# Kernel tuning notes

Hardware: AMD Instinct MI355X
Metric: run time of the kernel (lower is better)

Reference implementation:

```python
import jax, jax.numpy as jnp
import numpy as np


def _radon(img, angles, nBins):
    """Parallel-beam forward projection of a single [n, n] image.

    For each angle theta and detector bin s, integrate along the ray
    p = s*(cos,sin) + t*(-sin,cos) using bilinear interpolation with
    zero outside the image. Step size = 1 pixel, nSteps = n.
    Returns sinogram [nViews, nBins].
    """
    n = img.shape[-1]
    c = (n - 1) / 2.0
    s = jnp.arange(nBins, dtype=jnp.float32) - (nBins - 1) / 2.0  # detector coords
    t = jnp.arange(n, dtype=jnp.float32) - (n - 1) / 2.0          # integration param

    def samp(xi, yi):
        valid = (xi >= 0) & (xi < n) & (yi >= 0) & (yi < n)
        xi = jnp.clip(xi, 0, n - 1)
        yi = jnp.clip(yi, 0, n - 1)
        return jnp.where(valid, img[yi, xi], 0.0)

    def per_angle(theta):
        ct, st = jnp.cos(theta), jnp.sin(theta)
        # sample coordinates [nBins, nSteps]
        x = s[:, None] * ct - t[None, :] * st + c
        y = s[:, None] * st + t[None, :] * ct + c
        x0 = jnp.floor(x)
        y0 = jnp.floor(y)
        wx = x - x0
        wy = y - y0
        x0i = x0.astype(jnp.int32)
        y0i = y0.astype(jnp.int32)
        v = (samp(x0i, y0i) * (1 - wx) * (1 - wy)
             + samp(x0i + 1, y0i) * wx * (1 - wy)
             + samp(x0i, y0i + 1) * (1 - wx) * wy
             + samp(x0i + 1, y0i + 1) * wx * wy)
        return v.sum(axis=1)  # ray integral -> [nBins]

    # lax.map over angles keeps per-angle interpolation buffers small
    return jax.lax.map(per_angle, angles)  # [nViews, nBins]


def setup_inputs() -> dict:
    key = jax.random.key(0)
    x = jax.random.normal(key, (4, 1, 512, 512), dtype=jnp.float32)
    return {"x": x, "nViews": 512, "nBins": 512}


def reference(x, nViews, nBins):
    angles = jnp.arange(nViews, dtype=jnp.float32) * (np.pi / nViews)
    img = x[:, 0]  # [B, n, n]
    sino = jax.vmap(lambda im: _radon(im, angles, nBins))(img)  # [B, nViews, nBins]
    return sino[:, None, :, :]
```

## Files before the change

kernel.cpp:

```cpp
#include <hip/hip_runtime.h>


#define N_IMG 512
#define N_VIEWS 512
#define N_BINS 512
#define SB 64
#define TC 32
#define NCH (N_IMG / TC)
#define TDY 76
#define TDX 80
#define PITCH 81
#define GPR (TDX / 4)
#define NGRAN (TDY * GPR)

__global__ __launch_bounds__(256) void radon_fp_tiled4(const float* __restrict__ img,
                                                       float* __restrict__ out) {
    __shared__ float tile[TDY * PITCH];
    __shared__ float red[4][SB];

    const int v     = blockIdx.x;
    const int b     = blockIdx.y;
    const int stile = blockIdx.z;
    const int tid   = threadIdx.x;
    const int binl  = tid & 63;
    const int g     = tid >> 6;

    const float dth = (float)(3.14159265358979323846 / (double)N_VIEWS);
    float st, ct;
    sincosf((float)v * dth, &st, &ct);

    const float c = (float)(N_IMG - 1) * 0.5f;
    const float s = (float)(stile * SB + binl) - (float)(N_BINS - 1) * 0.5f;

    const float* __restrict__ im = img + (size_t)b * (N_IMG * N_IMG);

    const float sA  = (float)(stile * SB) - (float)(N_BINS - 1) * 0.5f;
    const float sBv = sA + (float)(SB - 1);

    float acc = 0.0f;

    for (int ch = 0; ch < NCH; ++ch) {
        const float tA = (float)(ch * TC) - (float)(N_IMG - 1) * 0.5f;
        const float tB = tA + (float)(TC - 1);

        const float xs[4] = { sA * ct - tA * st, sA * ct - tB * st,
                              sBv * ct - tA * st, sBv * ct - tB * st };
        const float ys[4] = { sA * st + tA * ct, sA * st + tB * ct,
                              sBv * st + tA * ct, sBv * st + tB * ct };
        const float xmin = fminf(fminf(xs[0], xs[1]), fminf(xs[2], xs[3])) + c;
        const float ymin = fminf(fminf(ys[0], ys[1]), fminf(ys[2], ys[3])) + c;
        const int X0 = ((int)floorf(xmin) - 1) & ~3;
        const int Y0 = (int)floorf(ymin) - 1;

        __syncthreads();

        const bool interior = (X0 >= 0) & (X0 + TDX <= N_IMG) &
                              (Y0 >= 0) & (Y0 + TDY <= N_IMG);
        if (interior) {
#pragma unroll
            for (int k = 0; k < 6; ++k) {
                const int gi = tid + k * 256;
                if (k < 5 || gi < NGRAN) {
                    const int r  = gi / GPR;
                    const int c4 = (gi - r * GPR) * 4;
                    const float4 vv = *reinterpret_cast<const float4*>(
                        im + ((Y0 + r) << 9) + X0 + c4);
                    float* dst = &tile[r * PITCH + c4];
                    dst[0] = vv.x; dst[1] = vv.y; dst[2] = vv.z; dst[3] = vv.w;
                }
            }
        } else {
#pragma unroll
            for (int k = 0; k < 6; ++k) {
                const int gi = tid + k * 256;
                if (k < 5 || gi < NGRAN) {
                    const int r  = gi / GPR;
                    const int c4 = (gi - r * GPR) * 4;
                    const int gy = Y0 + r;
                    const bool rowok = ((unsigned)gy < (unsigned)N_IMG);
                    float* dst = &tile[r * PITCH + c4];
#pragma unroll
                    for (int q = 0; q < 4; ++q) {
                        const int gx = X0 + c4 + q;
                        float val = 0.0f;
                        if (rowok && (unsigned)gx < (unsigned)N_IMG)
                            val = im[(gy << 9) + gx];
                        dst[q] = val;
                    }
                }
            }
        }
        __syncthreads();

        const float xbase = fmaf(s, ct, c - (float)X0);
        const float ybase = fmaf(s, st, c - (float)Y0);
        const float tb0 = (float)(ch * TC + g * 8) - (float)(N_IMG - 1) * 0.5f;
        const float xg = fmaf(-tb0, st, xbase);
        const float yg = fmaf(tb0, ct, ybase);
#pragma unroll
        for (int j = 0; j < 8; ++j) {
            const float xl = fmaf(-(float)j, st, xg);
            const float yl = fmaf((float)j, ct, yg);
            const float x0 = floorf(xl);
            const float y0 = floorf(yl);
            const float wx = xl - x0;
            const float wy = yl - y0;
            const int e = (int)fmaf(y0, (float)PITCH, x0);
            const float* p = &tile[e];
            const float v00 = p[0];
            const float v10 = p[1];
            const float v01 = p[PITCH];
            const float v11 = p[PITCH + 1];
            const float a0 = fmaf(v10 - v00, wx, v00);
            const float a1 = fmaf(v11 - v01, wx, v01);
            acc += fmaf(a1 - a0, wy, a0);
        }
    }

    red[g][binl] = acc;
    __syncthreads();
    if (tid < SB) {
        const float r0 = red[0][tid] + red[1][tid] + red[2][tid] + red[3][tid];
        out[((size_t)(b * N_VIEWS + v) << 9) + stile * SB + tid] = r0;
    }
}

extern "C" void kernel_launch(void* const* d_in, const int* in_sizes, int n_in,
                              void* d_out, int out_size, void* d_ws, size_t ws_size,
                              hipStream_t stream) {
    const float* img = (const float*)d_in[0];
    float* out = (float*)d_out;
    const int B = in_sizes[0] / (N_IMG * N_IMG);
    dim3 grid(N_VIEWS, B, N_BINS / SB);
    radon_fp_tiled4<<<grid, 256, 0, stream>>>(img, out);
}
```

Before: 688.8 us.

## Remap threads to 2D bin-by-step patches and reduce with wave shuffles

Each wavefront now covers 16 bins by 8 step offsets: a lane handles two bins, 8 apart, and strided steps, instead of one bin with 8 consecutive steps. This keeps a wave's LDS gathers within a compact 2D footprint, which is meant to cut LDS bank conflicts and add ILP through two independent accumulators. The final reduction uses cross-lane shuffles instead of a shared-memory array and an extra barrier. The tile-load index math is also simplified into fixed row/column splits with no division. The new thread mapping makes the access pattern depend on angle in a different way, which could help some views and hurt others.

```diff
diff --git a/kernel.cpp b/kernel.cpp
--- a/kernel.cpp
+++ b/kernel.cpp
@@ -10,34 +10,38 @@
 #define TDY 76
 #define TDX 80
 #define PITCH 81
-#define GPR (TDX / 4)
-#define NGRAN (TDY * GPR)
 
-__global__ __launch_bounds__(256) void radon_fp_tiled4(const float* __restrict__ img,
+__global__ __launch_bounds__(256) void radon_fp_tiled5(const float* __restrict__ img,
                                                        float* __restrict__ out) {
     __shared__ float tile[TDY * PITCH];
-    __shared__ float red[4][SB];
 
     const int v     = blockIdx.x;
     const int b     = blockIdx.y;
     const int stile = blockIdx.z;
     const int tid   = threadIdx.x;
-    const int binl  = tid & 63;
-    const int g     = tid >> 6;
+    const int lane  = tid & 63;
+    const int w     = tid >> 6;
+    const int ls    = lane & 7;
+    const int lt    = lane >> 3;
 
     const float dth = (float)(3.14159265358979323846 / (double)N_VIEWS);
     float st, ct;
     sincosf((float)v * dth, &st, &ct);
 
     const float c = (float)(N_IMG - 1) * 0.5f;
-    const float s = (float)(stile * SB + binl) - (float)(N_BINS - 1) * 0.5f;
+    const float s0 = (float)(stile * SB + w * 16 + ls) - (float)(N_BINS - 1) * 0.5f;
 
     const float* __restrict__ im = img + (size_t)b * (N_IMG * N_IMG);
 
     const float sA  = (float)(stile * SB) - (float)(N_BINS - 1) * 0.5f;
     const float sBv = sA + (float)(SB - 1);
 
-    float acc = 0.0f;
+    const int rA = tid >> 4;
+    const int gA = tid & 15;
+    const int rB = tid >> 2;
+    const int gB = 16 + (tid & 3);
+
+    float acc0 = 0.0f, acc1 = 0.0f;
 
     for (int ch = 0; ch < NCH; ++ch) {
         const float tA = (float)(ch * TC) - (float)(N_IMG - 1) * 0.5f;
@@ -58,30 +62,53 @@
                               (Y0 >= 0) & (Y0 + TDY <= N_IMG);
         if (interior) {
 #pragma unroll
-            for (int k = 0; k < 6; ++k) {
-                const int gi = tid + k * 256;
-                if (k < 5 || gi < NGRAN) {
-                    const int r  = gi / GPR;
-                    const int c4 = (gi - r * GPR) * 4;
+            for (int k = 0; k < 5; ++k) {
+                const int r = rA + k * 16;
+                if (k < 4 || r < TDY) {
                     const float4 vv = *reinterpret_cast<const float4*>(
-                        im + ((Y0 + r) << 9) + X0 + c4);
-                    float* dst = &tile[r * PITCH + c4];
+                        im + ((Y0 + r) << 9) + X0 + 4 * gA);
+                    float* dst = &tile[r * PITCH + 4 * gA];
+                    dst[0] = vv.x; dst[1] = vv.y; dst[2] = vv.z; dst[3] = vv.w;
+                }
+            }
+#pragma unroll
+            for (int k = 0; k < 2; ++k) {
+                const int r = rB + k * 64;
+                if (k == 0 || r < TDY) {
+                    const float4 vv = *reinterpret_cast<const float4*>(
+                        im + ((Y0 + r) << 9) + X0 + 4 * gB);
+                    float* dst = &tile[r * PITCH + 4 * gB];
                     dst[0] = vv.x; dst[1] = vv.y; dst[2] = vv.z; dst[3] = vv.w;
                 }
             }
         } else {
 #pragma unroll
-            for (int k = 0; k < 6; ++k) {
-                const int gi = tid + k * 256;
-                if (k < 5 || gi < NGRAN) {
-                    const int r  = gi / GPR;
-                    const int c4 = (gi - r * GPR) * 4;
+            for (int k = 0; k < 5; ++k) {
+                const int r = rA + k * 16;
+                if (k < 4 || r < TDY) {
                     const int gy = Y0 + r;
                     const bool rowok = ((unsigned)gy < (unsigned)N_IMG);
-                    float* dst = &tile[r * PITCH + c4];
+                    float* dst = &tile[r * PITCH + 4 * gA];
 #pragma unroll
                     for (int q = 0; q < 4; ++q) {
-                        const int gx = X0 + c4 + q;
+                        const int gx = X0 + 4 * gA + q;
+                        float val = 0.0f;
+                        if (rowok && (unsigned)gx < (unsigned)N_IMG)
+                            val = im[(gy << 9) + gx];
+                        dst[q] = val;
+                    }
+                }
+            }
+#pragma unroll
+            for (int k = 0; k < 2; ++k) {
+                const int r = rB + k * 64;
+                if (k == 0 || r < TDY) {
+                    const int gy = Y0 + r;
+                    const bool rowok = ((unsigned)gy < (unsigned)N_IMG);
+                    float* dst = &tile[r * PITCH + 4 * gB];
+#pragma unroll
+                    for (int q = 0; q < 4; ++q) {
+                        const int gx = X0 + 4 * gB + q;
                         float val = 0.0f;
                         if (rowok && (unsigned)gx < (unsigned)N_IMG)
                             val = im[(gy << 9) + gx];
@@ -92,36 +119,50 @@
         }
         __syncthreads();
 
-        const float xbase = fmaf(s, ct, c - (float)X0);
-        const float ybase = fmaf(s, st, c - (float)Y0);
-        const float tb0 = (float)(ch * TC + g * 8) - (float)(N_IMG - 1) * 0.5f;
-        const float xg = fmaf(-tb0, st, xbase);
-        const float yg = fmaf(tb0, ct, ybase);
+        const float cX = c - (float)X0;
+        const float cY = c - (float)Y0;
+        const float xg0 = fmaf(s0, ct, cX);
+        const float yg0 = fmaf(s0, st, cY);
+        const float xg1 = fmaf(8.0f, ct, xg0);
+        const float yg1 = fmaf(8.0f, st, yg0);
+        const float tb0 = (float)(ch * TC + lt) - (float)(N_IMG - 1) * 0.5f;
+        const float xa0 = fmaf(-tb0, st, xg0), ya0 = fmaf(tb0, ct, yg0);
+        const float xa1 = fmaf(-tb0, st, xg1), ya1 = fmaf(tb0, ct, yg1);
 #pragma unroll
-        for (int j = 0; j < 8; ++j) {
-            const float xl = fmaf(-(float)j, st, xg);
-            const float yl = fmaf((float)j, ct, yg);
-            const float x0 = floorf(xl);
-            const float y0 = floorf(yl);
-            const float wx = xl - x0;
-            const float wy = yl - y0;
-            const int e = (int)fmaf(y0, (float)PITCH, x0);
-            const float* p = &tile[e];
-            const float v00 = p[0];
-            const float v10 = p[1];
-            const float v01 = p[PITCH];
-            const float v11 = p[PITCH + 1];
-            const float a0 = fmaf(v10 - v00, wx, v00);
-            const float a1 = fmaf(v11 - v01, wx, v01);
-            acc += fmaf(a1 - a0, wy, a0);
+        for (int j = 0; j < 4; ++j) {
+            const float jj = (float)(8 * j);
+            {
+                const float xl = fmaf(-jj, st, xa0);
+                const float yl = fmaf(jj, ct, ya0);
+                const float x0 = floorf(xl), y0 = floorf(yl);
+                const float wx = xl - x0, wy = yl - y0;
+                const int e = (int)fmaf(y0, (float)PITCH, x0);
+                const float* p = &tile[e];
+                const float a0 = fmaf(p[1] - p[0], wx, p[0]);
+                const float a1 = fmaf(p[PITCH + 1] - p[PITCH], wx, p[PITCH]);
+                acc0 += fmaf(a1 - a0, wy, a0);
+            }
+            {
+                const float xl = fmaf(-jj, st, xa1);
+                const float yl = fmaf(jj, ct, ya1);
+                const float x0 = floorf(xl), y0 = floorf(yl);
+                const float wx = xl - x0, wy = yl - y0;
+                const int e = (int)fmaf(y0, (float)PITCH, x0);
+                const float* p = &tile[e];
+                const float a0 = fmaf(p[1] - p[0], wx, p[0]);
+                const float a1 = fmaf(p[PITCH + 1] - p[PITCH], wx, p[PITCH]);
+                acc1 += fmaf(a1 - a0, wy, a0);
+            }
         }
     }
 
-    red[g][binl] = acc;
-    __syncthreads();
-    if (tid < SB) {
-        const float r0 = red[0][tid] + red[1][tid] + red[2][tid] + red[3][tid];
-        out[((size_t)(b * N_VIEWS + v) << 9) + stile * SB + tid] = r0;
+    acc0 += __shfl_xor(acc0, 8);  acc0 += __shfl_xor(acc0, 16);  acc0 += __shfl_xor(acc0, 32);
+    acc1 += __shfl_xor(acc1, 8);  acc1 += __shfl_xor(acc1, 16);  acc1 += __shfl_xor(acc1, 32);
+
+    if (lane < 16) {
+        const float val = (lane < 8) ? acc0 : acc1;
+        const int bin = stile * SB + w * 16 + (lane & 7) + (lane & 8);
+        out[((size_t)(b * N_VIEWS + v) << 9) + bin] = val;
     }
 }
 
@@ -132,5 +173,5 @@
     float* out = (float*)d_out;
     const int B = in_sizes[0] / (N_IMG * N_IMG);
     dim3 grid(N_VIEWS, B, N_BINS / SB);
-    radon_fp_tiled4<<<grid, 256, 0, stream>>>(img, out);
+    radon_fp_tiled5<<<grid, 256, 0, stream>>>(img, out);
 }
```

Measured after the change: 647.7 us. 6.0% less time.
